# Kernel tuning notes

Measured on AMD Instinct MI355X. Metric: run time of the kernel, lower is better.

Reference implementation:

```python
import jax, jax.numpy as jnp
import numpy as np

_IDENTITY = jnp.array([1, 0, 0, 0], dtype=jnp.float32)

G, T, P, B = 512, 128, 256, 512  # num_graphs, max_terms, n_params, batch


def setup_inputs() -> dict:
    key = jax.random.key(0)
    k0, k1, k2, k3, k4 = jax.random.split(key, 5)
    psi_const = jax.random.randint(k0, (G, T), 0, 2).astype(jnp.int32)
    psi_params = jax.random.randint(k1, (G, T, P), 0, 2).astype(jnp.float32)
    phi_const = jax.random.randint(k2, (G, T), 0, 2).astype(jnp.int32)
    phi_params = jax.random.randint(k3, (G, T, P), 0, 2).astype(jnp.float32)
    param_vals = jax.random.randint(k4, (B, P), 0, 2).astype(jnp.float32)
    return {
        "psi_const": psi_const,
        "psi_params": psi_params,
        "phi_const": phi_const,
        "phi_params": phi_params,
        "param_vals": param_vals,
    }


def reference(psi_const, psi_params, phi_const, phi_params, param_vals):
    # GF(2) matmul: contract bitmasks with binary parameter values, mod 2.
    # psi_params: (G,T,P), param_vals: (B,P) -> (B,G,T)
    psi = jnp.mod(psi_const[None].astype(jnp.float32)
                  + jnp.einsum("gtp,bp->bgt", psi_params, param_vals), 2.0)
    phi = jnp.mod(phi_const[None].astype(jnp.float32)
                  + jnp.einsum("gtp,bp->bgt", phi_params, param_vals), 2.0)
    # Elementwise parity product and mod-2 sum over terms -> (B,G)
    exponent = jnp.mod(psi * phi, 2.0)
    sum_exponents = jnp.mod(jnp.sum(exponent, axis=-1), 2.0)
    # Parity-to-sign: (-1)^e = 1 - 2e, embedded as exact scalar (B,G,4)
    summands_exact = (1.0 - 2.0 * sum_exponents)[..., None] * _IDENTITY
    return summands_exact
```

## Files before the change

### kernel.cpp

```cpp
#include <hip/hip_runtime.h>

typedef unsigned long long u64;

#define G 512
#define T 128
#define P 256
#define B 512

struct __align__(16) U64x2 { u64 x, y; };

__global__ __launch_bounds__(256) void pack_pv_kernel(
    const float* __restrict__ pv, u64* __restrict__ out)
{
    int lane = threadIdx.x & 63;
    int wave = threadIdx.x >> 6;
    int row  = blockIdx.x * 4 + wave;
    const float4* src = (const float4*)(pv + (size_t)row * P);
    float4 f = src[lane];
    u64 w0 = __ballot(f.x != 0.0f);
    u64 w1 = __ballot(f.y != 0.0f);
    u64 w2 = __ballot(f.z != 0.0f);
    u64 w3 = __ballot(f.w != 0.0f);
    if (lane == 0) {
        out[row * 4 + 0] = w0;
        out[row * 4 + 1] = w1;
        out[row * 4 + 2] = w2;
        out[row * 4 + 3] = w3;
    }
}

__global__ __launch_bounds__(512) void pi_main_kernel(
    const int*   __restrict__ psi_const,
    const float* __restrict__ psi_params,
    const int*   __restrict__ phi_const,
    const float* __restrict__ phi_params,
    const u64*   __restrict__ pv,
    float4*      __restrict__ out)
{
    __shared__ __align__(16) u64 rows[T * 8];
    __shared__ unsigned code_sm[T];

    const int g    = blockIdx.x;
    const int tid  = threadIdx.x;
    const int lane = tid & 63;
    const int wave = tid >> 6;

    if (tid < T) {
        unsigned pc = ((unsigned)psi_const[g * T + tid]) & 1u;
        unsigned qc = ((unsigned)phi_const[g * T + tid]) & 1u;
        code_sm[tid] = pc | (qc << 1);
    }

    for (int i = 0; i < 32; ++i) {
        int r = wave * 32 + i;
        int t = r & (T - 1);
        const float* mat = (r < T) ? psi_params : phi_params;
        int off = (r < T) ? 0 : 4;
        const float4* src = (const float4*)(mat + ((size_t)g * T + t) * P);
        float4 f = src[lane];
        u64 w0 = __ballot(f.x != 0.0f);
        u64 w1 = __ballot(f.y != 0.0f);
        u64 w2 = __ballot(f.z != 0.0f);
        u64 w3 = __ballot(f.w != 0.0f);
        if (lane == 0) {
            U64x2* d = (U64x2*)&rows[t * 8 + off];
            U64x2 a; a.x = w0; a.y = w1;
            U64x2 c; c.x = w2; c.y = w3;
            d[0] = a;
            d[1] = c;
        }
    }
    __syncthreads();

    const int b = tid;
    const u64* v = pv + (size_t)b * 4;
    u64 v0 = v[0], v1 = v[1], v2 = v[2], v3 = v[3];

    unsigned e = 0;
    #pragma unroll 8
    for (int t = 0; t < T; ++t) {
        const U64x2* row = (const U64x2*)&rows[t * 8];
        U64x2 p0 = row[0], p1 = row[1], q0 = row[2], q1 = row[3];
        u64 ma = (p0.x & v0) ^ (p0.y & v1) ^ (p1.x & v2) ^ (p1.y & v3);
        u64 mb = (q0.x & v0) ^ (q0.y & v1) ^ (q1.x & v2) ^ (q1.y & v3);
        unsigned c = code_sm[t];
        e ^= (((unsigned)__popcll(ma) ^ c) & ((unsigned)__popcll(mb) ^ (c >> 1)));
    }
    e &= 1u;

    float s = 1.0f - 2.0f * (float)e;
    out[(size_t)b * G + g] = make_float4(s, 0.0f, 0.0f, 0.0f);
}

extern "C" void kernel_launch(void* const* d_in, const int* in_sizes, int n_in,
                              void* d_out, int out_size, void* d_ws, size_t ws_size,
                              hipStream_t stream) {
    const int*   psi_const  = (const int*)  d_in[0];
    const float* psi_params = (const float*)d_in[1];
    const int*   phi_const  = (const int*)  d_in[2];
    const float* phi_params = (const float*)d_in[3];
    const float* param_vals = (const float*)d_in[4];

    u64* pv_packed = (u64*)d_ws;

    pack_pv_kernel<<<B / 4, 256, 0, stream>>>(param_vals, pv_packed);
    pi_main_kernel<<<G, 512, 0, stream>>>(psi_const, psi_params,
                                          phi_const, phi_params,
                                          pv_packed, (float4*)d_out);
}
```

Measured before the change: 181.8 us.

## Split bit-packing of all parameter rows into a separate wide pack kernel

Moves the packing of psi/phi parameter rows out of the per-graph main kernel into a dedicated grid-wide pack kernel that writes packed bitmasks and term codes to workspace. The main kernel then reads the packed rows from global memory (uniform, cache-friendly loads) and is split into two 256-thread blocks per graph. This is meant to spread the heavy float-to-bit ballot work across many more waves and shorten the main kernel's serial prologue, at the cost of an extra workspace round trip and dependence on workspace being large enough, with a fallback to the old path otherwise.

```diff
diff --git a/kernel.cpp b/kernel.cpp
--- a/kernel.cpp
+++ b/kernel.cpp
@@ -6,6 +6,93 @@
 #define T 128
 #define P 256
 #define B 512
+
+#define PV_OFF    0
+#define ROWS_OFF  16384
+#define CODES_OFF (ROWS_OFF + (size_t)G * T * 8 * 8)
+#define WS_NEEDED (CODES_OFF + (size_t)G * T * 4)
+
+
+#define ROWS_TOTAL (G * T * 2)
+#define TASKS      (ROWS_TOTAL + B)
+#define TPW        16
+#define PACK_BLOCKS (TASKS / (TPW * 4))
+
+__global__ __launch_bounds__(256) void pack_all_kernel(
+    const int*   __restrict__ psi_const,
+    const float* __restrict__ psi_params,
+    const int*   __restrict__ phi_const,
+    const float* __restrict__ phi_params,
+    const float* __restrict__ pv,
+    u64*         __restrict__ rows_ws,
+    unsigned*    __restrict__ codes_ws,
+    u64*         __restrict__ pv_ws)
+{
+    int gtid = blockIdx.x * 256 + threadIdx.x;
+    if (gtid < G * T) {
+        unsigned pc = ((unsigned)psi_const[gtid]) & 1u;
+        unsigned qc = ((unsigned)phi_const[gtid]) & 1u;
+        codes_ws[gtid] = pc | (qc << 1);
+    }
+
+    const int lane = threadIdx.x & 63;
+    const int wv   = (blockIdx.x << 2) | (threadIdx.x >> 6);
+    const int base = wv * TPW;
+
+    for (int i = 0; i < TPW; ++i) {
+        int task = base + i;
+        const float* src;
+        u64* dst;
+        if (task < ROWS_TOTAL) {
+            int mat = task >> 16;
+            int idx = task & (G * T - 1);
+            src = (mat ? phi_params : psi_params) + (size_t)idx * P;
+            dst = rows_ws + (size_t)idx * 8 + mat * 4;
+        } else {
+            int b = task - ROWS_TOTAL;
+            src = pv + (size_t)b * P;
+            dst = pv_ws + (size_t)b * 4;
+        }
+        float4 f = ((const float4*)src)[lane];
+        u64 w0 = __ballot(f.x != 0.0f);
+        u64 w1 = __ballot(f.y != 0.0f);
+        u64 w2 = __ballot(f.z != 0.0f);
+        u64 w3 = __ballot(f.w != 0.0f);
+        if (lane == 0) {
+            dst[0] = w0; dst[1] = w1; dst[2] = w2; dst[3] = w3;
+        }
+    }
+}
+
+__global__ __launch_bounds__(256) void pi_main2_kernel(
+    const u64*      __restrict__ rows,
+    const unsigned* __restrict__ codes,
+    const u64*      __restrict__ pv,
+    float4*         __restrict__ out)
+{
+    const int g = blockIdx.x >> 1;
+    const int b = ((blockIdx.x & 1) << 8) | threadIdx.x;
+
+    const u64* v = pv + (size_t)b * 4;
+    u64 v0 = v[0], v1 = v[1], v2 = v[2], v3 = v[3];
+
+    const u64*      Rg = rows  + (size_t)g * (T * 8);
+    const unsigned* Cg = codes + g * T;
+
+    unsigned e = 0;
+    #pragma unroll 4
+    for (int t = 0; t < T; ++t) {
+        const u64* r = Rg + t * 8;
+        u64 ma = (r[0] & v0) ^ (r[1] & v1) ^ (r[2] & v2) ^ (r[3] & v3);
+        u64 mb = (r[4] & v0) ^ (r[5] & v1) ^ (r[6] & v2) ^ (r[7] & v3);
+        unsigned c = Cg[t];
+        e ^= (((unsigned)__popcll(ma) ^ c) & ((unsigned)__popcll(mb) ^ (c >> 1)));
+    }
+    e &= 1u;
+
+    float s = 1.0f - 2.0f * (float)e;
+    out[(size_t)b * G + g] = make_float4(s, 0.0f, 0.0f, 0.0f);
+}
 
 struct __align__(16) U64x2 { u64 x, y; };
 
@@ -101,10 +188,21 @@
     const float* phi_params = (const float*)d_in[3];
     const float* param_vals = (const float*)d_in[4];
 
-    u64* pv_packed = (u64*)d_ws;
-
-    pack_pv_kernel<<<B / 4, 256, 0, stream>>>(param_vals, pv_packed);
-    pi_main_kernel<<<G, 512, 0, stream>>>(psi_const, psi_params,
-                                          phi_const, phi_params,
-                                          pv_packed, (float4*)d_out);
-}
+    if (ws_size >= WS_NEEDED) {
+        u64*      pv_ws    = (u64*)((char*)d_ws + PV_OFF);
+        u64*      rows_ws  = (u64*)((char*)d_ws + ROWS_OFF);
+        unsigned* codes_ws = (unsigned*)((char*)d_ws + CODES_OFF);
+
+        pack_all_kernel<<<PACK_BLOCKS, 256, 0, stream>>>(
+            psi_const, psi_params, phi_const, phi_params, param_vals,
+            rows_ws, codes_ws, pv_ws);
+        pi_main2_kernel<<<G * 2, 256, 0, stream>>>(
+            rows_ws, codes_ws, pv_ws, (float4*)d_out);
+    } else {
+        u64* pv_packed = (u64*)d_ws;
+        pack_pv_kernel<<<B / 4, 256, 0, stream>>>(param_vals, pv_packed);
+        pi_main_kernel<<<G, 512, 0, stream>>>(psi_const, psi_params,
+                                              phi_const, phi_params,
+                                              pv_packed, (float4*)d_out);
+    }
+}
```

Result: slower. 194.1 us (+6.8%).

## Restructure GF(2) kernel: term-per-lane registers, linear bit packing, batch-uniform loads

Applied to the files above, without the earlier changes.

Replaces the ballot-based packing with per-thread scalar packing of 64 consecutive floats into a u64. This makes the packed bit order linear and is used both for param_vals and for the psi/phi rows in LDS. The main kernel now keeps two terms per lane in registers and loops over batch rows through wave-uniform loads. Per-term parities go into a bitmask and are reduced across the wave with xor shuffles, instead of each thread looping over all 128 terms from LDS. The aim is to cut LDS traffic and the serial per-thread term loop. The cost is more register pressure, a shuffle reduction, and each thread reading 256 bytes in contiguous uint4 loads.

```diff
diff --git a/kernel.cpp b/kernel.cpp
--- a/kernel.cpp
+++ b/kernel.cpp
@@ -6,6 +6,123 @@
 #define T 128
 #define P 256
 #define B 512
+
+#define WS_NEEDED 16384
+
+
+__device__ __forceinline__ unsigned nzbit(unsigned u) {
+    return (u | (0u - u)) >> 31;
+}
+
+__device__ __forceinline__ u64 pack64(const uint4* sv) {
+    uint4 f[16];
+    #pragma unroll
+    for (int i = 0; i < 16; ++i) f[i] = sv[i];
+    __builtin_amdgcn_sched_barrier(0);
+    unsigned lo = 0, hi = 0;
+    #pragma unroll
+    for (int i = 0; i < 8; ++i) {
+        lo |= nzbit(f[i].x) << (4 * i + 0);
+        lo |= nzbit(f[i].y) << (4 * i + 1);
+        lo |= nzbit(f[i].z) << (4 * i + 2);
+        lo |= nzbit(f[i].w) << (4 * i + 3);
+    }
+    #pragma unroll
+    for (int i = 8; i < 16; ++i) {
+        hi |= nzbit(f[i].x) << (4 * (i - 8) + 0);
+        hi |= nzbit(f[i].y) << (4 * (i - 8) + 1);
+        hi |= nzbit(f[i].z) << (4 * (i - 8) + 2);
+        hi |= nzbit(f[i].w) << (4 * (i - 8) + 3);
+    }
+    return ((u64)hi << 32) | (u64)lo;
+}
+
+__global__ __launch_bounds__(256) void pack_pv_linear_kernel(
+    const float* __restrict__ pv, u64* __restrict__ out)
+{
+    int tid = blockIdx.x * 256 + threadIdx.x;
+    out[tid] = pack64((const uint4*)(pv + (size_t)tid * 64));
+}
+
+#define LSTR 9
+
+__global__ __launch_bounds__(512, 4) void pi_fused_kernel(
+    const int*   __restrict__ psi_const,
+    const int*   __restrict__ phi_const,
+    const float* __restrict__ psi_params,
+    const float* __restrict__ phi_params,
+    const u64*   __restrict__ pv,
+    float4*      __restrict__ out)
+{
+    __shared__ u64 lds[T * LSTR];
+
+    const int g    = blockIdx.x;
+    const int tid  = threadIdx.x;
+    const int lane = tid & 63;
+    const int wv   = tid >> 6;
+
+    const size_t rowbase = (size_t)g * T * P;
+
+    #pragma unroll
+    for (int rep = 0; rep < 2; ++rep) {
+        int w    = rep * 512 + tid;
+        int t    = w >> 3;
+        int slot = w & 7;
+        int mat  = slot >> 2;
+        int j    = slot & 3;
+        const float* s = (mat ? phi_params : psi_params)
+                         + rowbase + (size_t)t * P + j * 64;
+        lds[t * LSTR + slot] = pack64((const uint4*)s);
+    }
+    __syncthreads();
+
+    u64 ra[8], rb[8];
+    #pragma unroll
+    for (int k = 0; k < 8; ++k) ra[k] = lds[lane * LSTR + k];
+    #pragma unroll
+    for (int k = 0; k < 8; ++k) rb[k] = lds[(lane + 64) * LSTR + k];
+
+    unsigned pa = ((unsigned)psi_const[g * T + lane]) & 1u;
+    unsigned qa = ((unsigned)phi_const[g * T + lane]) & 1u;
+    unsigned pb = ((unsigned)psi_const[g * T + lane + 64]) & 1u;
+    unsigned qb = ((unsigned)phi_const[g * T + lane + 64]) & 1u;
+
+    #pragma unroll
+    for (int grp = 0; grp < 2; ++grp) {
+        int b0  = wv * 64 + grp * 32;
+        int b0u = __builtin_amdgcn_readfirstlane(b0);
+        const u64* vp = pv + (size_t)b0u * 4;
+
+        unsigned acc = 0;
+        #pragma unroll
+        for (int i = 0; i < 32; ++i) {
+            u64 v0 = vp[i * 4 + 0], v1 = vp[i * 4 + 1];
+            u64 v2 = vp[i * 4 + 2], v3 = vp[i * 4 + 3];
+            u64 m0 = (ra[0] & v0) ^ (ra[1] & v1) ^ (ra[2] & v2) ^ (ra[3] & v3);
+            u64 m1 = (ra[4] & v0) ^ (ra[5] & v1) ^ (ra[6] & v2) ^ (ra[7] & v3);
+            u64 m2 = (rb[0] & v0) ^ (rb[1] & v1) ^ (rb[2] & v2) ^ (rb[3] & v3);
+            u64 m3 = (rb[4] & v0) ^ (rb[5] & v1) ^ (rb[6] & v2) ^ (rb[7] & v3);
+            unsigned f0 = (unsigned)m0 ^ (unsigned)(m0 >> 32);
+            unsigned f1 = (unsigned)m1 ^ (unsigned)(m1 >> 32);
+            unsigned f2 = (unsigned)m2 ^ (unsigned)(m2 >> 32);
+            unsigned f3 = (unsigned)m3 ^ (unsigned)(m3 >> 32);
+            unsigned t01 = ((unsigned)__popc(f0) ^ pa) & ((unsigned)__popc(f1) ^ qa);
+            unsigned t23 = ((unsigned)__popc(f2) ^ pb) & ((unsigned)__popc(f3) ^ qb);
+            acc ^= ((t01 ^ t23) & 1u) << i;
+        }
+
+        unsigned red = acc;
+        #pragma unroll
+        for (int m = 1; m < 64; m <<= 1)
+            red ^= __shfl_xor(red, m, 64);
+
+        if (lane < 32) {
+            int b = b0u + lane;
+            float s = 1.0f - 2.0f * (float)((red >> lane) & 1u);
+            out[(size_t)b * G + g] = make_float4(s, 0.0f, 0.0f, 0.0f);
+        }
+    }
+}
 
 struct __align__(16) U64x2 { u64 x, y; };
 
@@ -101,10 +218,18 @@
     const float* phi_params = (const float*)d_in[3];
     const float* param_vals = (const float*)d_in[4];
 
-    u64* pv_packed = (u64*)d_ws;
-
-    pack_pv_kernel<<<B / 4, 256, 0, stream>>>(param_vals, pv_packed);
-    pi_main_kernel<<<G, 512, 0, stream>>>(psi_const, psi_params,
-                                          phi_const, phi_params,
-                                          pv_packed, (float4*)d_out);
-}
+    u64* pv_ws = (u64*)d_ws;
+
+    if (ws_size >= WS_NEEDED) {
+        pack_pv_linear_kernel<<<(B * P / 64) / 256, 256, 0, stream>>>(
+            param_vals, pv_ws);
+        pi_fused_kernel<<<G, 512, 0, stream>>>(
+            psi_const, phi_const, psi_params, phi_params,
+            pv_ws, (float4*)d_out);
+    } else {
+        pack_pv_kernel<<<B / 4, 256, 0, stream>>>(param_vals, pv_ws);
+        pi_main_kernel<<<G, 512, 0, stream>>>(psi_const, psi_params,
+                                              phi_const, phi_params,
+                                              pv_ws, (float4*)d_out);
+    }
+}
```

Result: slower. 186.6 us (+2.6%).
